# Optimization experiments

Hardware: AMD Instinct MI355X
Metric: run time of the kernel (lower is better)

The kernel has to match this reference:

```python
import jax, jax.numpy as jnp
import numpy as np

INPUT_SIZE = 128
HIDDEN_SIZE = 128
OUTPUT_SIZE = 67  # hardcoded in the original module
SEQ_LEN = 512
BATCH = 2048


def setup_inputs() -> dict:
    key = jax.random.key(0)
    ks = jax.random.split(key, 7)
    x = jax.random.normal(ks[0], (INPUT_SIZE, SEQ_LEN, BATCH), dtype=jnp.float32)
    hidden = jax.random.normal(ks[1], (HIDDEN_SIZE, BATCH), dtype=jnp.float32)
    # bernoulli(0.5) mask applied column-wise to the initial hidden state
    drop_mask = jax.random.bernoulli(ks[2], 0.5, (HIDDEN_SIZE, BATCH)).astype(jnp.float32)
    # small init scale so tanh does not saturate
    Wi2h = jax.random.normal(ks[3], (HIDDEN_SIZE, INPUT_SIZE + HIDDEN_SIZE), dtype=jnp.float32) * 0.05
    bi2h = jax.random.normal(ks[4], (HIDDEN_SIZE,), dtype=jnp.float32) * 0.05
    Wi2o = jax.random.normal(ks[5], (OUTPUT_SIZE, HIDDEN_SIZE), dtype=jnp.float32) * 0.05
    bi2o = jax.random.normal(ks[6], (OUTPUT_SIZE,), dtype=jnp.float32) * 0.05
    return {"x": x, "hidden": hidden, "drop_mask": drop_mask,
            "Wi2h": Wi2h, "bi2h": bi2h, "Wi2o": Wi2o, "bi2o": bi2o}


def reference(x, hidden, drop_mask, Wi2h, bi2h, Wi2o, bi2o):
    # x: [input_size, seq_len, batch]; hidden: [hidden_size, batch]
    h0 = hidden * drop_mask  # per-column bernoulli dropout on initial state
    xs = jnp.transpose(x, (1, 0, 2))  # [seq, input_size, batch]

    def step(h, x_t):
        # combined = cat([x_t, h], dim=0).T -> [batch, input+hidden]
        combined = jnp.concatenate([x_t, h], axis=0).T
        h_new = jnp.tanh(combined @ Wi2h.T + bi2h)        # [batch, hidden]
        out = jax.nn.relu(h_new @ Wi2o.T + bi2o)          # [batch, output]
        return h_new.T, out.T                             # carry [hidden, batch], y [output, batch]

    _, ys = jax.lax.scan(step, h0, xs)  # ys: [seq, output, batch]
    Y = jnp.transpose(ys, (1, 0, 2))    # [output, seq, batch]
    return Y
```

## Files before the change

kernel.cpp:

```cpp
#include <hip/hip_runtime.h>
#include <hip/hip_bf16.h>
#include <stdint.h>

#define IN_SZ 128
#define HID 128
#define OUT_SZ 67
#define SEQ 512
#define BATCH 2048
#define BT 8
#define NTHR 640
#define SB (SEQ * BATCH)

typedef __attribute__((ext_vector_type(4))) float f32x4;
typedef __attribute__((ext_vector_type(8))) short s16x8;
typedef __attribute__((ext_vector_type(8))) __bf16 bf16x8;

static __device__ __forceinline__ unsigned short f2bf(float f) {
  union { float f; uint32_t u; } c; c.f = f;
  uint32_t u = c.u;
  uint32_t r = u + 0x7FFFu + ((u >> 16) & 1u);
  return (unsigned short)(r >> 16);
}
static __device__ __forceinline__ uint32_t pk2bf(float lo, float hi) {
  __hip_bfloat162 h2 = __float22bfloat162_rn(float2{lo, hi});
  union { __hip_bfloat162 h; uint32_t u; } c; c.h = h2;
  return c.u;
}
static __device__ __forceinline__ float fast_tanh(float x) {
  float e = __builtin_amdgcn_exp2f(x * 2.885390081777927f);
  float r = __builtin_amdgcn_rcpf(e + 1.f);
  return __builtin_fmaf(-2.f, r, 1.f);
}
static __device__ __forceinline__ void mfma16(f32x4& c, s16x8 a, s16x8 b) {
  c = __builtin_amdgcn_mfma_f32_16x16x32_bf16(
        __builtin_bit_cast(bf16x8, a), __builtin_bit_cast(bf16x8, b), c, 0, 0, 0);
}
#define KOFF(g, j) (4 * (g) + ((j) & 3) + (((j) >> 2) << 4))

static __device__ __forceinline__ void frag_barrier() {
  __builtin_amdgcn_sched_barrier(0);
  asm volatile("s_waitcnt lgkmcnt(0)");
  __builtin_amdgcn_s_barrier();
  __builtin_amdgcn_sched_barrier(0);
}

__global__ __launch_bounds__(NTHR, 1) void rnn_kernel(
    const float* __restrict__ x, const float* __restrict__ hidden,
    const float* __restrict__ mask, const float* __restrict__ Wi2h,
    const float* __restrict__ bi2h, const float* __restrict__ Wi2o,
    const float* __restrict__ bi2o, float* __restrict__ Y) {

  __shared__ s16x8 sF[2][8][64];

  const int tid = threadIdx.x;
  const int wave = tid >> 6;
  const int lane = tid & 63;
  const int g = lane >> 4;
  const int n16 = lane & 15;
  const int bid = ((blockIdx.x & 7) << 5) | (blockIdx.x >> 3);
  const int b0 = bid * BT;

  if (wave < 8) {
    s16x8 W[8];
#pragma unroll
    for (int kt = 0; kt < 8; ++kt) {
      const float* wr = Wi2h + (size_t)(16 * wave + n16) * (IN_SZ + HID);
      s16x8 w8;
#pragma unroll
      for (int j = 0; j < 8; ++j)
        w8[j] = (short)f2bf(wr[32 * kt + KOFF(g, j)]);
      W[kt] = w8;
    }
    f32x4 bhv;
#pragma unroll
    for (int r = 0; r < 4; ++r) bhv[r] = bi2h[16 * wave + 4 * g + r];

    const int lc = tid & 7;
    const int lrb = tid >> 3;
    const int R0 = 2 * lrb;
    const int skk = R0 >> 5;
    const int r5 = R0 & 31;
    const int sg = (r5 < 16) ? (r5 >> 2) : ((r5 - 16) >> 2);
    const int sq = ((r5 & 2) >> 1) + ((r5 < 16) ? 0 : 2);
    const int slane = (sg << 4) | lc;
    const char* const xB = (const char*)x;
    const uint32_t xrb0 = ((uint32_t)R0 * (uint32_t)SB + (uint32_t)(b0 + lc)) * 4u;
    const uint32_t xrb1 = ((uint32_t)(R0 + 1) * (uint32_t)SB + (uint32_t)(b0 + lc)) * 4u;

    {
      float v0 = *(const float*)(xB + xrb0);
      float v1 = *(const float*)(xB + xrb1);
      ((uint32_t*)&sF[0][skk][slane])[sq] = pk2bf(v0, v1);
      uint32_t h0o = (uint32_t)R0 * (uint32_t)BATCH + (uint32_t)(b0 + lc);
      uint32_t h1o = (uint32_t)(R0 + 1) * (uint32_t)BATCH + (uint32_t)(b0 + lc);
      float hv0 = hidden[(size_t)h0o] * mask[(size_t)h0o];
      float hv1 = hidden[(size_t)h1o] * mask[(size_t)h1o];
      ((uint32_t*)&sF[0][4 + skk][slane])[sq] = pk2bf(hv0, hv1);
    }
    float xq0[2], xq1[2], xq2[2], xq3[2];
    xq0[0] = *(const float*)(xB + xrb0 + 1u * BATCH * 4u);
    xq0[1] = *(const float*)(xB + xrb1 + 1u * BATCH * 4u);
    xq1[0] = *(const float*)(xB + xrb0 + 2u * BATCH * 4u);
    xq1[1] = *(const float*)(xB + xrb1 + 2u * BATCH * 4u);
    xq2[0] = *(const float*)(xB + xrb0 + 3u * BATCH * 4u);
    xq2[1] = *(const float*)(xB + xrb1 + 3u * BATCH * 4u);
    xq3[0] = *(const float*)(xB + xrb0 + 4u * BATCH * 4u);
    xq3[1] = *(const float*)(xB + xrb1 + 4u * BATCH * 4u);
    frag_barrier();

    uint32_t* const hdst0 = (uint32_t*)&sF[0][4 + (wave >> 1)][lane] + (wave & 1) * 2;
    uint32_t* const hdst1 = (uint32_t*)&sF[1][4 + (wave >> 1)][lane] + (wave & 1) * 2;

#define STEPC(T, P, XQ)                                                         \
  {                                                                             \
    const int t = (T);                                                          \
    const int pn = (P) ^ 1;                                                     \
               \
    ((uint32_t*)&sF[pn][skk][slane])[sq] = pk2bf(XQ[0], XQ[1]);                 \
    {                                                                           \
      const uint32_t tn = (uint32_t)((t + 5 > 511) ? 511 : t + 5) * (BATCH * 4u); \
      XQ[0] = *(const float*)(xB + xrb0 + tn);                                  \
      XQ[1] = *(const float*)(xB + xrb1 + tn);                                  \
    }                                                                           \
                                           \
    s16x8 X0 = sF[P][0][lane], X1 = sF[P][1][lane];                             \
    s16x8 X2 = sF[P][2][lane], X3 = sF[P][3][lane];                             \
    s16x8 H0 = sF[P][4][lane], H1 = sF[P][5][lane];                             \
    s16x8 H2 = sF[P][6][lane], H3 = sF[P][7][lane];                             \
                                      \
    f32x4 a = bhv, a2 = {0.f, 0.f, 0.f, 0.f};                                   \
    f32x4 ax = {0.f, 0.f, 0.f, 0.f}, ax2 = {0.f, 0.f, 0.f, 0.f};                \
    mfma16(a, W[4], H0);   mfma16(a2, W[5], H1);                                \
    mfma16(ax, W[0], X0);  mfma16(ax2, W[1], X1);                               \
    mfma16(a, W[6], H2);   mfma16(a2, W[7], H3);                                \
    mfma16(ax, W[2], X2);  mfma16(ax2, W[3], X3);                               \
        \
    {                                                                           \
      f32x4 s0 = (a + a2) + (ax + ax2);                                         \
      uint32_t hp[2];                                                           \
      hp[0] = pk2bf(fast_tanh(s0[0]), fast_tanh(s0[1]));                        \
      hp[1] = pk2bf(fast_tanh(s0[2]), fast_tanh(s0[3]));                        \
      *(uint64_t*)(pn ? hdst1 : hdst0) = *(uint64_t*)hp;                        \
    }                                                                           \
    frag_barrier();                                                             \
  }

    for (int t4 = 0; t4 < SEQ; t4 += 4) {
      STEPC(t4 + 0, 0, xq0)
      STEPC(t4 + 1, 1, xq1)
      STEPC(t4 + 2, 0, xq2)
      STEPC(t4 + 3, 1, xq3)
    }
#undef STEPC

  } else {
    const int ow = wave - 8;
    s16x8 wO[3][4];
    f32x4 bov[3];
    uint32_t ybase[3];
    bool tvalid[3];
#pragma unroll
    for (int ot = 0; ot < 3; ++ot) {
      const int tk = 3 * ow + ot;
      tvalid[ot] = (tk < 5);
#pragma unroll
      for (int kk = 0; kk < 4; ++kk) {
        s16x8 a;
#pragma unroll
        for (int j = 0; j < 8; ++j) {
          int m = 16 * tk + n16;
          a[j] = (short)((tvalid[ot] && m < OUT_SZ)
                         ? f2bf(Wi2o[(size_t)m * HID + 32 * kk + KOFF(g, j)]) : 0);
        }
        wO[ot][kk] = a;
      }
#pragma unroll
      for (int r = 0; r < 4; ++r) {
        int m = 16 * tk + 4 * g + r;
        bov[ot][r] = (tvalid[ot] && m < OUT_SZ) ? bi2o[m] : 0.f;
      }
      ybase[ot] = (uint32_t)(16 * tk + 4 * g) * (uint32_t)SB + (uint32_t)(b0 + n16);
    }

    frag_barrier();
    frag_barrier();

    for (int t = 1; t < SEQ; ++t) {
      const int P = t & 1;
      s16x8 H0 = sF[P][4][lane], H1 = sF[P][5][lane];
      s16x8 H2 = sF[P][6][lane], H3 = sF[P][7][lane];
      const uint32_t ty = (uint32_t)(t - 1) * (uint32_t)BATCH;
#pragma unroll
      for (int ot = 0; ot < 3; ++ot) {
        if (tvalid[ot]) {
          const int tk = 3 * ow + ot;
          f32x4 ao = bov[ot];
          mfma16(ao, wO[ot][0], H0); mfma16(ao, wO[ot][1], H1);
          mfma16(ao, wO[ot][2], H2); mfma16(ao, wO[ot][3], H3);
          if (n16 < BT) {
#pragma unroll
            for (int r = 0; r < 4; ++r)
              if (16 * tk + 4 * g + r < OUT_SZ)
                Y[(size_t)(ybase[ot] + (uint32_t)r * SB + ty)] = fmaxf(ao[r], 0.f);
          }
        }
      }
      frag_barrier();
    }
    {
      s16x8 H0 = sF[0][4][lane], H1 = sF[0][5][lane];
      s16x8 H2 = sF[0][6][lane], H3 = sF[0][7][lane];
      const uint32_t ty = 511u * (uint32_t)BATCH;
#pragma unroll
      for (int ot = 0; ot < 3; ++ot) {
        if (tvalid[ot]) {
          const int tk = 3 * ow + ot;
          f32x4 ao = bov[ot];
          mfma16(ao, wO[ot][0], H0); mfma16(ao, wO[ot][1], H1);
          mfma16(ao, wO[ot][2], H2); mfma16(ao, wO[ot][3], H3);
          if (n16 < BT) {
#pragma unroll
            for (int r = 0; r < 4; ++r)
              if (16 * tk + 4 * g + r < OUT_SZ)
                Y[(size_t)(ybase[ot] + (uint32_t)r * SB + ty)] = fmaxf(ao[r], 0.f);
          }
        }
      }
    }
  }
}

extern "C" void kernel_launch(void* const* d_in, const int* in_sizes, int n_in,
                              void* d_out, int out_size, void* d_ws, size_t ws_size,
                              hipStream_t stream) {
  const float* x      = (const float*)d_in[0];
  const float* hidden = (const float*)d_in[1];
  const float* mask   = (const float*)d_in[2];
  const float* Wi2h   = (const float*)d_in[3];
  const float* bi2h   = (const float*)d_in[4];
  const float* Wi2o   = (const float*)d_in[5];
  const float* bi2o   = (const float*)d_in[6];
  float* Y = (float*)d_out;
  (void)in_sizes; (void)n_in; (void)out_size; (void)d_ws; (void)ws_size;
  rnn_kernel<<<dim3(BATCH / BT), dim3(NTHR), 0, stream>>>(
      x, hidden, mask, Wi2h, bi2h, Wi2o, bi2o, Y);
}
```

Before: 518.4 us.

## Offload x staging to dedicated side waves with triple-buffered LDS

The x-loading and bf16 packing work moves out of the 8 recurrence waves into the side waves, which now number 4 (block grows to 768 threads). x gets a triple-buffered LDS region separate from the double-buffered hidden state, and the prefetch distance grows to 8 steps. The output projection is spread over 3 of the 4 side waves as 2/2/1 tiles, and the fourth does only loading. The aim is to shorten the serial critical path of the recurrence waves by removing global loads and LDS stores from it. The cost is more waves taking part in every barrier and more register use for the prefetch queues.

```diff
diff --git a/kernel.cpp b/kernel.cpp
--- a/kernel.cpp
+++ b/kernel.cpp
@@ -8,7 +8,7 @@
 #define SEQ 512
 #define BATCH 2048
 #define BT 8
-#define NTHR 640
+#define NTHR 768
 #define SB (SEQ * BATCH)
 
 typedef __attribute__((ext_vector_type(4))) float f32x4;
@@ -50,7 +50,8 @@
     const float* __restrict__ bi2h, const float* __restrict__ Wi2o,
     const float* __restrict__ bi2o, float* __restrict__ Y) {
 
-  __shared__ s16x8 sF[2][8][64];
+  __shared__ s16x8 sX[3][4][64];
+  __shared__ s16x8 sH[2][4][64];
 
   const int tid = threadIdx.x;
   const int wave = tid >> 6;
@@ -75,101 +76,61 @@
 #pragma unroll
     for (int r = 0; r < 4; ++r) bhv[r] = bi2h[16 * wave + 4 * g + r];
 
-    const int lc = tid & 7;
-    const int lrb = tid >> 3;
-    const int R0 = 2 * lrb;
-    const int skk = R0 >> 5;
-    const int r5 = R0 & 31;
-    const int sg = (r5 < 16) ? (r5 >> 2) : ((r5 - 16) >> 2);
-    const int sq = ((r5 & 2) >> 1) + ((r5 < 16) ? 0 : 2);
-    const int slane = (sg << 4) | lc;
-    const char* const xB = (const char*)x;
-    const uint32_t xrb0 = ((uint32_t)R0 * (uint32_t)SB + (uint32_t)(b0 + lc)) * 4u;
-    const uint32_t xrb1 = ((uint32_t)(R0 + 1) * (uint32_t)SB + (uint32_t)(b0 + lc)) * 4u;
-
-    {
-      float v0 = *(const float*)(xB + xrb0);
-      float v1 = *(const float*)(xB + xrb1);
-      ((uint32_t*)&sF[0][skk][slane])[sq] = pk2bf(v0, v1);
-      uint32_t h0o = (uint32_t)R0 * (uint32_t)BATCH + (uint32_t)(b0 + lc);
-      uint32_t h1o = (uint32_t)(R0 + 1) * (uint32_t)BATCH + (uint32_t)(b0 + lc);
-      float hv0 = hidden[(size_t)h0o] * mask[(size_t)h0o];
-      float hv1 = hidden[(size_t)h1o] * mask[(size_t)h1o];
-      ((uint32_t*)&sF[0][4 + skk][slane])[sq] = pk2bf(hv0, hv1);
-    }
-    float xq0[2], xq1[2], xq2[2], xq3[2];
-    xq0[0] = *(const float*)(xB + xrb0 + 1u * BATCH * 4u);
-    xq0[1] = *(const float*)(xB + xrb1 + 1u * BATCH * 4u);
-    xq1[0] = *(const float*)(xB + xrb0 + 2u * BATCH * 4u);
-    xq1[1] = *(const float*)(xB + xrb1 + 2u * BATCH * 4u);
-    xq2[0] = *(const float*)(xB + xrb0 + 3u * BATCH * 4u);
-    xq2[1] = *(const float*)(xB + xrb1 + 3u * BATCH * 4u);
-    xq3[0] = *(const float*)(xB + xrb0 + 4u * BATCH * 4u);
-    xq3[1] = *(const float*)(xB + xrb1 + 4u * BATCH * 4u);
     frag_barrier();
 
-    uint32_t* const hdst0 = (uint32_t*)&sF[0][4 + (wave >> 1)][lane] + (wave & 1) * 2;
-    uint32_t* const hdst1 = (uint32_t*)&sF[1][4 + (wave >> 1)][lane] + (wave & 1) * 2;
-
-#define STEPC(T, P, XQ)                                                         \
+    uint32_t* const hdst0 = (uint32_t*)&sH[0][wave >> 1][lane] + (wave & 1) * 2;
+    uint32_t* const hdst1 = (uint32_t*)&sH[1][wave >> 1][lane] + (wave & 1) * 2;
+
+#define CSTEP(K)                                                                \
   {                                                                             \
-    const int t = (T);                                                          \
-    const int pn = (P) ^ 1;                                                     \
-               \
-    ((uint32_t*)&sF[pn][skk][slane])[sq] = pk2bf(XQ[0], XQ[1]);                 \
-    {                                                                           \
-      const uint32_t tn = (uint32_t)((t + 5 > 511) ? 511 : t + 5) * (BATCH * 4u); \
-      XQ[0] = *(const float*)(xB + xrb0 + tn);                                  \
-      XQ[1] = *(const float*)(xB + xrb1 + tn);                                  \
-    }                                                                           \
-                                           \
-    s16x8 X0 = sF[P][0][lane], X1 = sF[P][1][lane];                             \
-    s16x8 X2 = sF[P][2][lane], X3 = sF[P][3][lane];                             \
-    s16x8 H0 = sF[P][4][lane], H1 = sF[P][5][lane];                             \
-    s16x8 H2 = sF[P][6][lane], H3 = sF[P][7][lane];                             \
-                                      \
+    const int P = (K) & 1;                                                      \
+    const int S = (K) % 3;                                                      \
+    s16x8 H0 = sH[P][0][lane], H1 = sH[P][1][lane];                             \
+    s16x8 H2 = sH[P][2][lane], H3 = sH[P][3][lane];                             \
+    s16x8 X0 = sX[S][0][lane], X1 = sX[S][1][lane];                             \
+    s16x8 X2 = sX[S][2][lane], X3 = sX[S][3][lane];                             \
     f32x4 a = bhv, a2 = {0.f, 0.f, 0.f, 0.f};                                   \
     f32x4 ax = {0.f, 0.f, 0.f, 0.f}, ax2 = {0.f, 0.f, 0.f, 0.f};                \
     mfma16(a, W[4], H0);   mfma16(a2, W[5], H1);                                \
     mfma16(ax, W[0], X0);  mfma16(ax2, W[1], X1);                               \
     mfma16(a, W[6], H2);   mfma16(a2, W[7], H3);                                \
     mfma16(ax, W[2], X2);  mfma16(ax2, W[3], X3);                               \
-        \
     {                                                                           \
       f32x4 s0 = (a + a2) + (ax + ax2);                                         \
       uint32_t hp[2];                                                           \
       hp[0] = pk2bf(fast_tanh(s0[0]), fast_tanh(s0[1]));                        \
       hp[1] = pk2bf(fast_tanh(s0[2]), fast_tanh(s0[3]));                        \
-      *(uint64_t*)(pn ? hdst1 : hdst0) = *(uint64_t*)hp;                        \
+      *(uint64_t*)(P ? hdst0 : hdst1) = *(uint64_t*)hp;                         \
     }                                                                           \
     frag_barrier();                                                             \
   }
 
-    for (int t4 = 0; t4 < SEQ; t4 += 4) {
-      STEPC(t4 + 0, 0, xq0)
-      STEPC(t4 + 1, 1, xq1)
-      STEPC(t4 + 2, 0, xq2)
-      STEPC(t4 + 3, 1, xq3)
-    }
-#undef STEPC
+    for (int t6 = 0; t6 < 510; t6 += 6) {
+      CSTEP(0) CSTEP(1) CSTEP(2) CSTEP(3) CSTEP(4) CSTEP(5)
+    }
+    CSTEP(0) CSTEP(1)
+#undef CSTEP
 
   } else {
-    const int ow = wave - 8;
-    s16x8 wO[3][4];
-    f32x4 bov[3];
-    uint32_t ybase[3];
-    bool tvalid[3];
-#pragma unroll
-    for (int ot = 0; ot < 3; ++ot) {
-      const int tk = 3 * ow + ot;
-      tvalid[ot] = (tk < 5);
+    const int sv = wave - 8;
+    const int svl = (sv << 6) | lane;
+
+    const int ntile = (sv < 2) ? 2 : (sv == 2 ? 1 : 0);
+    const int tk0 = 2 * sv;
+    s16x8 wO[2][4];
+    f32x4 bov[2];
+    uint32_t ybase[2];
+#pragma unroll
+    for (int ot = 0; ot < 2; ++ot) {
+      const int tk = tk0 + ot;
+      const bool tv = (ot < ntile);
 #pragma unroll
       for (int kk = 0; kk < 4; ++kk) {
         s16x8 a;
 #pragma unroll
         for (int j = 0; j < 8; ++j) {
           int m = 16 * tk + n16;
-          a[j] = (short)((tvalid[ot] && m < OUT_SZ)
+          a[j] = (short)((tv && m < OUT_SZ)
                          ? f2bf(Wi2o[(size_t)m * HID + 32 * kk + KOFF(g, j)]) : 0);
         }
         wO[ot][kk] = a;
@@ -177,44 +138,121 @@
 #pragma unroll
       for (int r = 0; r < 4; ++r) {
         int m = 16 * tk + 4 * g + r;
-        bov[ot][r] = (tvalid[ot] && m < OUT_SZ) ? bi2o[m] : 0.f;
+        bov[ot][r] = (tv && m < OUT_SZ) ? bi2o[m] : 0.f;
       }
       ybase[ot] = (uint32_t)(16 * tk + 4 * g) * (uint32_t)SB + (uint32_t)(b0 + n16);
     }
 
+    int skkA, sqA, slaneA, skkB, sqB, slaneB;
+    uint32_t xaA0, xaA1, xaB0, xaB1;
+    {
+      int d = 2 * svl;
+      int rp = d >> 3, lc = d & 7, R0 = 2 * rp;
+      int r5 = R0 & 31;
+      int sg = (r5 < 16) ? (r5 >> 2) : ((r5 - 16) >> 2);
+      skkA = R0 >> 5;
+      sqA = ((r5 & 2) >> 1) + ((r5 < 16) ? 0 : 2);
+      slaneA = (sg << 4) | lc;
+      xaA0 = ((uint32_t)R0 * (uint32_t)SB + (uint32_t)(b0 + lc)) * 4u;
+      xaA1 = ((uint32_t)(R0 + 1) * (uint32_t)SB + (uint32_t)(b0 + lc)) * 4u;
+      d = 2 * svl + 1;
+      rp = d >> 3; lc = d & 7; R0 = 2 * rp;
+      r5 = R0 & 31;
+      sg = (r5 < 16) ? (r5 >> 2) : ((r5 - 16) >> 2);
+      skkB = R0 >> 5;
+      sqB = ((r5 & 2) >> 1) + ((r5 < 16) ? 0 : 2);
+      slaneB = (sg << 4) | lc;
+      xaB0 = ((uint32_t)R0 * (uint32_t)SB + (uint32_t)(b0 + lc)) * 4u;
+      xaB1 = ((uint32_t)(R0 + 1) * (uint32_t)SB + (uint32_t)(b0 + lc)) * 4u;
+    }
+    const char* const xB = (const char*)x;
+
+#pragma unroll
+    for (int tt = 0; tt < 2; ++tt) {
+      const uint32_t to = (uint32_t)tt * (BATCH * 4u);
+      float a0 = *(const float*)(xB + xaA0 + to);
+      float a1 = *(const float*)(xB + xaA1 + to);
+      float c0 = *(const float*)(xB + xaB0 + to);
+      float c1 = *(const float*)(xB + xaB1 + to);
+      ((uint32_t*)&sX[tt][skkA][slaneA])[sqA] = pk2bf(a0, a1);
+      ((uint32_t*)&sX[tt][skkB][slaneB])[sqB] = pk2bf(c0, c1);
+    }
+    {
+      const uint32_t hA0 = (xaA0 / (4u * SB)) * (uint32_t)BATCH + (uint32_t)(b0 + ((2 * svl) & 7));
+      const uint32_t hA1 = (xaA1 / (4u * SB)) * (uint32_t)BATCH + (uint32_t)(b0 + ((2 * svl) & 7));
+      const uint32_t hB0 = (xaB0 / (4u * SB)) * (uint32_t)BATCH + (uint32_t)(b0 + ((2 * svl + 1) & 7));
+      const uint32_t hB1 = (xaB1 / (4u * SB)) * (uint32_t)BATCH + (uint32_t)(b0 + ((2 * svl + 1) & 7));
+      float a0 = hidden[(size_t)hA0] * mask[(size_t)hA0];
+      float a1 = hidden[(size_t)hA1] * mask[(size_t)hA1];
+      float c0 = hidden[(size_t)hB0] * mask[(size_t)hB0];
+      float c1 = hidden[(size_t)hB1] * mask[(size_t)hB1];
+      ((uint32_t*)&sH[0][skkA][slaneA])[sqA] = pk2bf(a0, a1);
+      ((uint32_t*)&sH[0][skkB][slaneB])[sqB] = pk2bf(c0, c1);
+    }
+    float q0[4], q1[4], q2[4], q3[4], q4[4], q5[4];
+#define FILLQ(Q, T)                                                             \
+    {                                                                           \
+      const uint32_t to = (uint32_t)(T) * (BATCH * 4u);                         \
+      Q[0] = *(const float*)(xB + xaA0 + to);                                   \
+      Q[1] = *(const float*)(xB + xaA1 + to);                                   \
+      Q[2] = *(const float*)(xB + xaB0 + to);                                   \
+      Q[3] = *(const float*)(xB + xaB1 + to);                                   \
+    }
+    FILLQ(q0, 2) FILLQ(q1, 3) FILLQ(q2, 4) FILLQ(q3, 5) FILLQ(q4, 6) FILLQ(q5, 7)
     frag_barrier();
-    frag_barrier();
-
-    for (int t = 1; t < SEQ; ++t) {
-      const int P = t & 1;
-      s16x8 H0 = sF[P][4][lane], H1 = sF[P][5][lane];
-      s16x8 H2 = sF[P][6][lane], H3 = sF[P][7][lane];
-      const uint32_t ty = (uint32_t)(t - 1) * (uint32_t)BATCH;
-#pragma unroll
-      for (int ot = 0; ot < 3; ++ot) {
-        if (tvalid[ot]) {
-          const int tk = 3 * ow + ot;
-          f32x4 ao = bov[ot];
-          mfma16(ao, wO[ot][0], H0); mfma16(ao, wO[ot][1], H1);
-          mfma16(ao, wO[ot][2], H2); mfma16(ao, wO[ot][3], H3);
-          if (n16 < BT) {
-#pragma unroll
-            for (int r = 0; r < 4; ++r)
-              if (16 * tk + 4 * g + r < OUT_SZ)
-                Y[(size_t)(ybase[ot] + (uint32_t)r * SB + ty)] = fmaxf(ao[r], 0.f);
-          }
-        }
-      }
-      frag_barrier();
+
+#define SSTEP(K, Q)                                                             \
+  {                                                                             \
+    const int t = t6 + (K);                                                     \
+    const int SW = ((K) + 2) % 3;                                               \
+    ((uint32_t*)&sX[SW][skkA][slaneA])[sqA] = pk2bf(Q[0], Q[1]);                \
+    ((uint32_t*)&sX[SW][skkB][slaneB])[sqB] = pk2bf(Q[2], Q[3]);                \
+    {                                                                           \
+      const int tn = (t + 8 > 511) ? 511 : t + 8;                               \
+      FILLQ(Q, tn)                                                              \
+    }                                                                           \
+    if (ntile > 0 && t > 0) {                                                   \
+      const int P = (K) & 1;                                                    \
+      s16x8 H0 = sH[P][0][lane], H1 = sH[P][1][lane];                           \
+      s16x8 H2 = sH[P][2][lane], H3 = sH[P][3][lane];                           \
+      const uint32_t ty = (uint32_t)(t - 1) * (uint32_t)BATCH;                  \
+      _Pragma("unroll")                                                         \
+      for (int ot = 0; ot < 2; ++ot) {                                          \
+        if (ot < ntile) {                                                       \
+          const int tk = tk0 + ot;                                              \
+          f32x4 ao = bov[ot];                                                   \
+          mfma16(ao, wO[ot][0], H0); mfma16(ao, wO[ot][1], H1);                 \
+          mfma16(ao, wO[ot][2], H2); mfma16(ao, wO[ot][3], H3);                 \
+          if (n16 < BT) {                                                       \
+            _Pragma("unroll")                                                   \
+            for (int r = 0; r < 4; ++r)                                         \
+              if (16 * tk + 4 * g + r < OUT_SZ)                                 \
+                Y[(size_t)(ybase[ot] + (uint32_t)r * SB + ty)] = fmaxf(ao[r], 0.f); \
+          }                                                                     \
+        }                                                                       \
+      }                                                                         \
+    }                                                                           \
+    frag_barrier();                                                             \
+  }
+
+    for (int t6 = 0; t6 < 510; t6 += 6) {
+      SSTEP(0, q0) SSTEP(1, q1) SSTEP(2, q2) SSTEP(3, q3) SSTEP(4, q4) SSTEP(5, q5)
     }
     {
-      s16x8 H0 = sF[0][4][lane], H1 = sF[0][5][lane];
-      s16x8 H2 = sF[0][6][lane], H3 = sF[0][7][lane];
+      const int t6 = 510;
+      SSTEP(0, q0) SSTEP(1, q1)
+    }
+#undef SSTEP
+#undef FILLQ
+
+    if (ntile > 0) {
+      s16x8 H0 = sH[0][0][lane], H1 = sH[0][1][lane];
+      s16x8 H2 = sH[0][2][lane], H3 = sH[0][3][lane];
       const uint32_t ty = 511u * (uint32_t)BATCH;
 #pragma unroll
-      for (int ot = 0; ot < 3; ++ot) {
-        if (tvalid[ot]) {
-          const int tk = 3 * ow + ot;
+      for (int ot = 0; ot < 2; ++ot) {
+        if (ot < ntile) {
+          const int tk = tk0 + ot;
           f32x4 ao = bov[ot];
           mfma16(ao, wO[ot][0], H0); mfma16(ao, wO[ot][1], H1);
           mfma16(ao, wO[ot][2], H2); mfma16(ao, wO[ot][3], H3);
```

Result: faster. 482.6 us (-6.9%).
